# Kernel tuning notes

Measured on AMD Instinct MI355X. Metric: run time of the kernel, lower is better.

## Reference

```python
import jax, jax.numpy as jnp
import numpy as np

EPS = 1e-12  # torch F.normalize default eps


def setup_inputs() -> dict:
    key = jax.random.key(0)
    k1, k2, k3 = jax.random.split(key, 3)
    ns, d_in, n_feat, n_classes = 16384, 512, 256, 1000
    x = jax.random.normal(k1, (ns, d_in), dtype=jnp.float32)
    W = jax.random.normal(k2, (d_in, n_feat), dtype=jnp.float32) * 0.05
    # class prototypes: L2-normalized embeddings, one per seen class (seen_c == n_classes)
    means = jax.random.normal(k3, (n_classes, n_feat), dtype=jnp.float32)
    means = means / jnp.maximum(jnp.linalg.norm(means, axis=1, keepdims=True), EPS)
    return {"x": x, "W": W, "means": means, "t": 0}


def reference(x, W, means, t):
    # forward_training: backbone + L2 normalization along feature dim
    feats = x @ W                                   # [ns, n_feat]
    preds = feats / jnp.maximum(jnp.linalg.norm(feats, axis=1, keepdims=True), EPS)
    # deployment forward: nearest prototype by negative dot product
    # original: per-sample dist = -means @ pred^T; dist.min(0) -> class index
    dist = -(preds @ means.T)                       # [ns, seen_c]
    classpred = jnp.argmin(dist, axis=1)            # first min on ties, matches torch
    n_classes = means.shape[0]
    out = jax.nn.one_hot(classpred, n_classes, dtype=jnp.float32)  # [ns, n_classes]
    return out
```

## Files before the change

kernel.cpp:

```cpp
#include <hip/hip_runtime.h>
#include <float.h>

#define NS   16384
#define K1   512
#define F    256
#define NC   1000
#define SPB  64
#define NTHR 512
#define NBLK (NS / SPB)


typedef _Float16 half8  __attribute__((ext_vector_type(8)));
typedef _Float16 half4v __attribute__((ext_vector_type(4)));
typedef float    float4v __attribute__((ext_vector_type(4)));

#define M_OFF 262144

#define PREP_BLKS 192
#define ZERO_BLKS 2048

__global__ void prep(const float* __restrict__ W, const float* __restrict__ means,
                     _Float16* __restrict__ ws, float* __restrict__ out) {
    const int bid = blockIdx.x;
    if (bid >= PREP_BLKS) {
        const size_t total4 = (size_t)NS * NC / 4;
        const float4v z4 = (float4v){0.f, 0.f, 0.f, 0.f};
        size_t base = (size_t)(bid - PREP_BLKS) * 2048 + threadIdx.x;
#pragma unroll
        for (int j = 0; j < 8; ++j) {
            size_t q = base + (size_t)j * 256;
            if (q < total4)
                __builtin_nontemporal_store(z4, reinterpret_cast<float4v*>(out) + q);
        }
        return;
    }
    int g = bid * blockDim.x + threadIdx.x;
    if (g < 16384) {
        int lane = g & 63, tile = g >> 6;
        int ks = tile >> 4, nt = tile & 15;
        int k0 = ks * 32 + (lane >> 4) * 8;
        int n  = nt * 16 + (lane & 15);
        half8 hv, lv;
#pragma unroll
        for (int j = 0; j < 8; ++j) {
            float v = W[(size_t)(k0 + j) * F + n] * 16.0f;
            _Float16 hi = (_Float16)v;
            hv[j] = hi;
            lv[j] = (_Float16)(v - (float)hi);
        }
        _Float16* d = ws + (size_t)tile * 1024 + (size_t)lane * 8;
        *reinterpret_cast<half8*>(d)       = hv;
        *reinterpret_cast<half8*>(d + 512) = lv;
    } else {
        int gm = g - 16384;
        int lane = gm & 63, tile = gm >> 6;
        int ks = tile >> 6, gt = tile & 63;
        int k0 = ks * 32 + (lane >> 4) * 8;
        int c  = gt * 16 + (lane & 15);
        half8 hv, lv;
#pragma unroll
        for (int j = 0; j < 8; ++j) {
            float v = (c < NC) ? means[(size_t)c * F + k0 + j] * 16.0f : 0.0f;
            _Float16 hi = (_Float16)v;
            hv[j] = hi;
            lv[j] = (_Float16)(v - (float)hi);
        }
        _Float16* d = ws + M_OFF + (size_t)tile * 1024 + (size_t)lane * 8;
        *reinterpret_cast<half8*>(d)       = hv;
        *reinterpret_cast<half8*>(d + 512) = lv;
    }
}

#define MFMA(a, b, c) __builtin_amdgcn_mfma_f32_16x16x32_f16((a), (b), (c), 0, 0, 0)

__device__ __forceinline__ void vmwait(int n) {
    switch (n) {
        case 0: asm volatile("s_waitcnt vmcnt(0)" ::: "memory"); break;
        case 2: asm volatile("s_waitcnt vmcnt(2)" ::: "memory"); break;
        case 4: asm volatile("s_waitcnt vmcnt(4)" ::: "memory"); break;
        default: asm volatile("s_waitcnt vmcnt(6)" ::: "memory"); break;
    }
    __builtin_amdgcn_sched_barrier(0);
}

#define FH_OFF  0
#define FL_OFF  16384
#define OVL_OFF 32768
#define SH_HALVES 65536

#define FH_P(r, c) (&SH[FH_OFF + ((r) << 8) + ((c) ^ (((r) & 7) << 3))])
#define FL_P(r, c) (&SH[FL_OFF + ((r) << 8) + ((c) ^ (((r) & 7) << 3))])
#define XS_IDX(r, c) ((((r) >> 1) << 6) + ((((((r) & 1) << 5)) + (c)) ^ ((((r) >> 1) & 7) << 3)))
#define XSH_P(b, r, c) (&SH[OVL_OFF + (b) * 2048 + XS_IDX(r, c)])
#define XSL_P(b, r, c) (&SH[OVL_OFF + 4096 + (b) * 2048 + XS_IDX(r, c)])

__attribute__((amdgpu_flat_work_group_size(NTHR, NTHR), amdgpu_waves_per_eu(2, 4)))
__global__ void fused_mfma(const float* __restrict__ x,
                           const _Float16* __restrict__ ws,
                           float* __restrict__ out) {
    __shared__ _Float16 SH[SH_HALVES];
    __shared__ float cand_v[64][8];
    __shared__ int   cand_i[64][8];
    __shared__ int   bidx[64];

    const int tid  = threadIdx.x;
    const int lane = tid & 63;
    const int w    = tid >> 6;
    const int quad = lane >> 4;
    const int cl   = lane & 15;
    const int s0   = blockIdx.x * SPB;

    const int xrow = tid >> 3;
    const int xc4  = (tid & 7) * 4;

    float4v acc1[2][4];
#pragma unroll
    for (int p = 0; p < 2; ++p)
#pragma unroll
        for (int mt = 0; mt < 4; ++mt)
            acc1[p][mt] = (float4v){0.f, 0.f, 0.f, 0.f};

    const _Float16* wsrc = ws + ((size_t)(w * 2) << 10) + ((size_t)lane << 3);
    half8 wbh[2][2], wbl[2][2];
#pragma unroll
    for (int p = 0; p < 2; ++p) {
        wbh[0][p] = *reinterpret_cast<const half8*>(wsrc + p * 1024);
        wbl[0][p] = *reinterpret_cast<const half8*>(wsrc + p * 1024 + 512);
    }

    float4v xv = *reinterpret_cast<const float4v*>(x + (size_t)(s0 + xrow) * K1 + xc4);

#define P1_BODY(k, buf) do {                                                   \
        { half4v hx, lx;                                                       \
          _Pragma("unroll") for (int j = 0; j < 4; ++j) {                      \
              float v = xv[j] * 8.0f; _Float16 hi = (_Float16)v;               \
              hx[j] = hi; lx[j] = (_Float16)(v - (float)hi); }                 \
          *reinterpret_cast<half4v*>(XSH_P(buf, xrow, xc4)) = hx;              \
          *reinterpret_cast<half4v*>(XSL_P(buf, xrow, xc4)) = lx; }            \
        __syncthreads();                                                       \
        if ((k) < 15)                                                          \
            xv = *reinterpret_cast<const float4v*>(                            \
                x + (size_t)(s0 + xrow) * K1 + ((k) + 1) * 32 + xc4);          \
        _Pragma("unroll") for (int p = 0; p < 2; ++p) {                        \
            wbh[(buf) ^ 1][p] = *reinterpret_cast<const half8*>(               \
                wsrc + (size_t)((k) + 1) * 16384 + p * 1024);                  \
            wbl[(buf) ^ 1][p] = *reinterpret_cast<const half8*>(               \
                wsrc + (size_t)((k) + 1) * 16384 + p * 1024 + 512); }          \
        half8 ah[4], al[4];                                                    \
        _Pragma("unroll") for (int mt = 0; mt < 4; ++mt) {                     \
            ah[mt] = *reinterpret_cast<const half8*>(                          \
                XSH_P(buf, mt * 16 + cl, quad * 8));                           \
            al[mt] = *reinterpret_cast<const half8*>(                          \
                XSL_P(buf, mt * 16 + cl, quad * 8)); }                         \
        __builtin_amdgcn_s_setprio(1);                                         \
        _Pragma("unroll") for (int p = 0; p < 2; ++p)                          \
            _Pragma("unroll") for (int mt = 0; mt < 4; ++mt) {                 \
                acc1[p][mt] = MFMA(ah[mt], wbh[buf][p], acc1[p][mt]);          \
                acc1[p][mt] = MFMA(ah[mt], wbl[buf][p], acc1[p][mt]);          \
                acc1[p][mt] = MFMA(al[mt], wbh[buf][p], acc1[p][mt]); }        \
        __builtin_amdgcn_s_setprio(0);                                         \
    } while (0)

    for (int k2 = 0; k2 < 8; ++k2) {
        P1_BODY(2 * k2, 0);
        P1_BODY(2 * k2 + 1, 1);
    }

#pragma unroll
    for (int p = 0; p < 2; ++p)
#pragma unroll
        for (int mt = 0; mt < 4; ++mt)
#pragma unroll
            for (int r = 0; r < 4; ++r) {
                int srow = mt * 16 + quad * 4 + r;
                int n    = (w * 2 + p) * 16 + cl;
                float v  = acc1[p][mt][r];
                _Float16 hi = (_Float16)v;
                *FH_P(srow, n) = hi;
                *FL_P(srow, n) = (_Float16)(v - (float)hi);
            }
    __syncthreads();

    float4v acc2[4][8];
#pragma unroll
    for (int mt = 0; mt < 4; ++mt)
#pragma unroll
        for (int c = 0; c < 8; ++c)
            acc2[mt][c] = (float4v){0.f, 0.f, 0.f, 0.f};

    _Float16* fifo = &SH[OVL_OFF + w * 4096];
    const _Float16* mg = ws + M_OFF + ((size_t)w << 10) + ((size_t)lane << 3);

#define STAGE_OFF(goff, slot) do {                                             \
        __builtin_amdgcn_global_load_lds(                                      \
            (const __attribute__((address_space(1))) void*)(mg + (goff)),      \
            (__attribute__((address_space(3))) void*)(fifo + (slot) * 1024),   \
            16, 0, 0);                                                         \
        __builtin_amdgcn_global_load_lds(                                      \
            (const __attribute__((address_space(1))) void*)(mg + (goff) + 512),\
            (__attribute__((address_space(3))) void*)(fifo + (slot) * 1024 + 512),\
            16, 0, 0);                                                         \
    } while (0)

#define LOAD_A(kk) do { int c0_ = (kk) * 32 + quad * 8;                        \
        _Pragma("unroll") for (int mt = 0; mt < 4; ++mt) {                     \
            fah[mt] = *reinterpret_cast<const half8*>(FH_P(mt * 16 + cl, c0_));\
            fal[mt] = *reinterpret_cast<const half8*>(FL_P(mt * 16 + cl, c0_));\
        } } while (0)

#define FB_READ(slot, rb) do {                                                 \
        const _Float16* sl_ = fifo + (slot) * 1024 + lane * 8;                 \
        fbh[rb] = *reinterpret_cast<const half8*>(sl_);                        \
        fbl[rb] = *reinterpret_cast<const half8*>(sl_ + 512);                  \
    } while (0)

#define MFMA12(gt, rb) do {                                                    \
        __builtin_amdgcn_s_setprio(1);                                         \
        _Pragma("unroll") for (int mt = 0; mt < 4; ++mt) {                     \
            acc2[mt][gt] = MFMA(fah[mt], fbh[rb], acc2[mt][gt]);               \
            acc2[mt][gt] = MFMA(fah[mt], fbl[rb], acc2[mt][gt]);               \
            acc2[mt][gt] = MFMA(fal[mt], fbh[rb], acc2[mt][gt]); }             \
        __builtin_amdgcn_s_setprio(0);                                         \
    } while (0)

    half8 fah[4], fal[4];
    half8 fbh[2], fbl[2];

    STAGE_OFF(0, 0); STAGE_OFF(8192, 1); STAGE_OFF(16384, 2);
    LOAD_A(0);
    vmwait(4);
    FB_READ(0, 0);

    for (int ks = 0; ks < 7; ++ks) {
#pragma unroll
        for (int gt = 0; gt < 8; ++gt) {
            if (gt < 5) STAGE_OFF((gt + 3) * 8192, (gt + 3) & 3);
            else        STAGE_OFF(65536 + (gt - 5) * 8192, (gt + 3) & 3);
            if (gt == 0 && ks > 0) LOAD_A(ks);
            vmwait(4);
            FB_READ((gt + 1) & 3, (gt + 1) & 1);
            MFMA12(gt, gt & 1);
        }
        mg += 65536;
    }
#pragma unroll
    for (int gt = 0; gt < 8; ++gt) {
        if (gt < 5) STAGE_OFF((gt + 3) * 8192, (gt + 3) & 3);
        if (gt == 0) LOAD_A(7);
        if (gt < 5)       vmwait(4);
        else if (gt == 5) vmwait(2);
        else if (gt == 6) vmwait(0);
        if (gt < 7) FB_READ((gt + 1) & 3, (gt + 1) & 1);
        MFMA12(gt, gt & 1);
    }

#pragma unroll
    for (int mt = 0; mt < 4; ++mt)
#pragma unroll
        for (int r = 0; r < 4; ++r) {
            float v  = -FLT_MAX;
            int   ix = 0x7FFFFFFF;
#pragma unroll
            for (int nt = 0; nt < 8; ++nt) {
                int c = (nt * 8 + w) * 16 + cl;
                if (c < NC) {
                    float sc = acc2[mt][nt][r];
                    if (sc > v) { v = sc; ix = c; }
                }
            }
#pragma unroll
            for (int off = 1; off < 16; off <<= 1) {
                float ov = __shfl_xor(v, off, 64);
                int   oi = __shfl_xor(ix, off, 64);
                if (ov > v || (ov == v && oi < ix)) { v = ov; ix = oi; }
            }
            if (cl == 0) {
                int srow = mt * 16 + quad * 4 + r;
                cand_v[srow][w] = v;
                cand_i[srow][w] = ix;
            }
        }
    __syncthreads();

    if (tid < SPB) {
        float v  = cand_v[tid][0];
        int   ix = cand_i[tid][0];
#pragma unroll
        for (int q = 1; q < 8; ++q) {
            float ov = cand_v[tid][q];
            int   oi = cand_i[tid][q];
            if (ov > v || (ov == v && oi < ix)) { v = ov; ix = oi; }
        }
        bidx[tid] = ix;
    }
    __syncthreads();

    if (tid < SPB)
        out[(size_t)(s0 + tid) * NC + bidx[tid]] = 1.0f;
}

extern "C" void kernel_launch(void* const* d_in, const int* in_sizes, int n_in,
                              void* d_out, int out_size, void* d_ws, size_t ws_size,
                              hipStream_t stream) {
    const float* x     = (const float*)d_in[0];
    const float* W     = (const float*)d_in[1];
    const float* means = (const float*)d_in[2];
    float* out         = (float*)d_out;
    _Float16* ws       = (_Float16*)d_ws;

    prep<<<PREP_BLKS + ZERO_BLKS, 256, 0, stream>>>(W, means, ws, out);
    fused_mfma<<<NBLK, NTHR, 0, stream>>>(x, ws, out);
}
```

Measured before the change: 138.5 us.

## Stage x in half-K chunks and restructure prototype pipeline with barriers

Phase 1 now loads and converts half of each x row (256 columns) into a larger swizzled LDS tile at once, so the per-k-step __syncthreads goes away and only one extra barrier per half remains. Phase 2 replaces the 4-slot per-wave FIFO with a double buffer holding two column tiles per stage. Each stage is bracketed by s_barrier so the waves stay in lockstep. The aim is to cut synchronization and the number of load-wait steps. The risks are a shallower prefetch depth and added workgroup-wide barriers in phase 2.

```diff
diff --git a/kernel.cpp b/kernel.cpp
--- a/kernel.cpp
+++ b/kernel.cpp
@@ -90,9 +90,8 @@
 
 #define FH_P(r, c) (&SH[FH_OFF + ((r) << 8) + ((c) ^ (((r) & 7) << 3))])
 #define FL_P(r, c) (&SH[FL_OFF + ((r) << 8) + ((c) ^ (((r) & 7) << 3))])
-#define XS_IDX(r, c) ((((r) >> 1) << 6) + ((((((r) & 1) << 5)) + (c)) ^ ((((r) >> 1) & 7) << 3)))
-#define XSH_P(b, r, c) (&SH[OVL_OFF + (b) * 2048 + XS_IDX(r, c)])
-#define XSL_P(b, r, c) (&SH[OVL_OFF + 4096 + (b) * 2048 + XS_IDX(r, c)])
+#define XH_P(r, c) (&SH[OVL_OFF + ((r) << 8) + ((c) ^ (((r) & 7) << 3))])
+#define XL_P(r, c) (&SH[OVL_OFF + 16384 + ((r) << 8) + ((c) ^ (((r) & 7) << 3))])
 
 __attribute__((amdgpu_flat_work_group_size(NTHR, NTHR), amdgpu_waves_per_eu(2, 4)))
 __global__ void fused_mfma(const float* __restrict__ x,
@@ -111,7 +110,7 @@
     const int s0   = blockIdx.x * SPB;
 
     const int xrow = tid >> 3;
-    const int xc4  = (tid & 7) * 4;
+    const int xk0  = (tid & 7) * 32;
 
     float4v acc1[2][4];
 #pragma unroll
@@ -128,42 +127,56 @@
         wbl[0][p] = *reinterpret_cast<const half8*>(wsrc + p * 1024 + 512);
     }
 
-    float4v xv = *reinterpret_cast<const float4v*>(x + (size_t)(s0 + xrow) * K1 + xc4);
-
-#define P1_BODY(k, buf) do {                                                   \
-        { half4v hx, lx;                                                       \
-          _Pragma("unroll") for (int j = 0; j < 4; ++j) {                      \
-              float v = xv[j] * 8.0f; _Float16 hi = (_Float16)v;               \
-              hx[j] = hi; lx[j] = (_Float16)(v - (float)hi); }                 \
-          *reinterpret_cast<half4v*>(XSH_P(buf, xrow, xc4)) = hx;              \
-          *reinterpret_cast<half4v*>(XSL_P(buf, xrow, xc4)) = lx; }            \
-        __syncthreads();                                                       \
-        if ((k) < 15)                                                          \
-            xv = *reinterpret_cast<const float4v*>(                            \
-                x + (size_t)(s0 + xrow) * K1 + ((k) + 1) * 32 + xc4);          \
-        _Pragma("unroll") for (int p = 0; p < 2; ++p) {                        \
-            wbh[(buf) ^ 1][p] = *reinterpret_cast<const half8*>(               \
-                wsrc + (size_t)((k) + 1) * 16384 + p * 1024);                  \
-            wbl[(buf) ^ 1][p] = *reinterpret_cast<const half8*>(               \
-                wsrc + (size_t)((k) + 1) * 16384 + p * 1024 + 512); }          \
+#define P1B(ksl, par) do {                                                     \
+        const int ks_ = h * 8 + (ksl);                                         \
+        if (ks_ < 15) {                                                        \
+            _Pragma("unroll") for (int p = 0; p < 2; ++p) {                    \
+                wbh[(par) ^ 1][p] = *reinterpret_cast<const half8*>(           \
+                    wsrc + (size_t)(ks_ + 1) * 16384 + p * 1024);              \
+                wbl[(par) ^ 1][p] = *reinterpret_cast<const half8*>(           \
+                    wsrc + (size_t)(ks_ + 1) * 16384 + p * 1024 + 512); } }    \
         half8 ah[4], al[4];                                                    \
         _Pragma("unroll") for (int mt = 0; mt < 4; ++mt) {                     \
             ah[mt] = *reinterpret_cast<const half8*>(                          \
-                XSH_P(buf, mt * 16 + cl, quad * 8));                           \
+                XH_P(mt * 16 + cl, (ksl) * 32 + quad * 8));                    \
             al[mt] = *reinterpret_cast<const half8*>(                          \
-                XSL_P(buf, mt * 16 + cl, quad * 8)); }                         \
+                XL_P(mt * 16 + cl, (ksl) * 32 + quad * 8)); }                  \
         __builtin_amdgcn_s_setprio(1);                                         \
         _Pragma("unroll") for (int p = 0; p < 2; ++p)                          \
             _Pragma("unroll") for (int mt = 0; mt < 4; ++mt) {                 \
-                acc1[p][mt] = MFMA(ah[mt], wbh[buf][p], acc1[p][mt]);          \
-                acc1[p][mt] = MFMA(ah[mt], wbl[buf][p], acc1[p][mt]);          \
-                acc1[p][mt] = MFMA(al[mt], wbh[buf][p], acc1[p][mt]); }        \
+                acc1[p][mt] = MFMA(ah[mt], wbh[par][p], acc1[p][mt]);          \
+                acc1[p][mt] = MFMA(ah[mt], wbl[par][p], acc1[p][mt]);          \
+                acc1[p][mt] = MFMA(al[mt], wbh[par][p], acc1[p][mt]); }        \
         __builtin_amdgcn_s_setprio(0);                                         \
     } while (0)
 
-    for (int k2 = 0; k2 < 8; ++k2) {
-        P1_BODY(2 * k2, 0);
-        P1_BODY(2 * k2 + 1, 1);
+    for (int h = 0; h < 2; ++h) {
+        if (h) __syncthreads();
+        {
+            const float* xp = x + (size_t)(s0 + xrow) * K1 + h * 256 + xk0;
+            float4v xv[8];
+#pragma unroll
+            for (int j = 0; j < 8; ++j)
+                xv[j] = *reinterpret_cast<const float4v*>(xp + j * 4);
+#pragma unroll
+            for (int j8 = 0; j8 < 4; ++j8) {
+                half8 hx, lx;
+#pragma unroll
+                for (int e = 0; e < 8; ++e) {
+                    float v = xv[j8 * 2 + (e >> 2)][e & 3] * 8.0f;
+                    _Float16 hi = (_Float16)v;
+                    hx[e] = hi;
+                    lx[e] = (_Float16)(v - (float)hi);
+                }
+                *reinterpret_cast<half8*>(XH_P(xrow, xk0 + j8 * 8)) = hx;
+                *reinterpret_cast<half8*>(XL_P(xrow, xk0 + j8 * 8)) = lx;
+            }
+        }
+        __syncthreads();
+        for (int k2 = 0; k2 < 4; ++k2) {
+            P1B(2 * k2, 0);
+            P1B(2 * k2 + 1, 1);
+        }
     }
 
 #pragma unroll
@@ -191,14 +204,14 @@
     _Float16* fifo = &SH[OVL_OFF + w * 4096];
     const _Float16* mg = ws + M_OFF + ((size_t)w << 10) + ((size_t)lane << 3);
 
-#define STAGE_OFF(goff, slot) do {                                             \
+#define STAGE2(goff, loff) do {                                                \
         __builtin_amdgcn_global_load_lds(                                      \
             (const __attribute__((address_space(1))) void*)(mg + (goff)),      \
-            (__attribute__((address_space(3))) void*)(fifo + (slot) * 1024),   \
+            (__attribute__((address_space(3))) void*)(fifo + (loff)),          \
             16, 0, 0);                                                         \
         __builtin_amdgcn_global_load_lds(                                      \
             (const __attribute__((address_space(1))) void*)(mg + (goff) + 512),\
-            (__attribute__((address_space(3))) void*)(fifo + (slot) * 1024 + 512),\
+            (__attribute__((address_space(3))) void*)(fifo + (loff) + 512),    \
             16, 0, 0);                                                         \
     } while (0)
 
@@ -208,50 +221,47 @@
             fal[mt] = *reinterpret_cast<const half8*>(FL_P(mt * 16 + cl, c0_));\
         } } while (0)
 
-#define FB_READ(slot, rb) do {                                                 \
-        const _Float16* sl_ = fifo + (slot) * 1024 + lane * 8;                 \
-        fbh[rb] = *reinterpret_cast<const half8*>(sl_);                        \
-        fbl[rb] = *reinterpret_cast<const half8*>(sl_ + 512);                  \
+#define MFMA12(gt, BH, BL) do {                                                \
+        _Pragma("unroll") for (int mt = 0; mt < 4; ++mt) {                     \
+            acc2[mt][gt] = MFMA(fah[mt], BH, acc2[mt][gt]);                    \
+            acc2[mt][gt] = MFMA(fah[mt], BL, acc2[mt][gt]);                    \
+            acc2[mt][gt] = MFMA(fal[mt], BH, acc2[mt][gt]); }                  \
     } while (0)
 
-#define MFMA12(gt, rb) do {                                                    \
+#define P2B(j4) do {                                                           \
+        if ((j4) < 3) {                                                        \
+            STAGE2((((j4) + 1) * 2)     * 8192, (((j4) + 1) & 1) * 2048);      \
+            STAGE2((((j4) + 1) * 2 + 1) * 8192, (((j4) + 1) & 1) * 2048 + 1024);\
+            vmwait(4);                                                         \
+        } else if (ks < 7) {                                                   \
+            STAGE2(65536,        (((j4) + 1) & 1) * 2048);                     \
+            STAGE2(65536 + 8192, (((j4) + 1) & 1) * 2048 + 1024);              \
+            vmwait(4);                                                         \
+        } else {                                                               \
+            vmwait(0);                                                         \
+        }                                                                      \
+        const _Float16* sl_ = fifo + ((j4) & 1) * 2048 + (size_t)lane * 8;     \
+        half8 b0h = *reinterpret_cast<const half8*>(sl_);                      \
+        half8 b0l = *reinterpret_cast<const half8*>(sl_ + 512);                \
+        half8 b1h = *reinterpret_cast<const half8*>(sl_ + 1024);               \
+        half8 b1l = *reinterpret_cast<const half8*>(sl_ + 1536);               \
+        if ((j4) == 0) LOAD_A(ks);                                             \
+        __builtin_amdgcn_s_barrier();                                          \
         __builtin_amdgcn_s_setprio(1);                                         \
-        _Pragma("unroll") for (int mt = 0; mt < 4; ++mt) {                     \
-            acc2[mt][gt] = MFMA(fah[mt], fbh[rb], acc2[mt][gt]);               \
-            acc2[mt][gt] = MFMA(fah[mt], fbl[rb], acc2[mt][gt]);               \
-            acc2[mt][gt] = MFMA(fal[mt], fbh[rb], acc2[mt][gt]); }             \
+        MFMA12((j4) * 2,     b0h, b0l);                                        \
+        MFMA12((j4) * 2 + 1, b1h, b1l);                                        \
         __builtin_amdgcn_s_setprio(0);                                         \
+        __builtin_amdgcn_s_barrier();                                          \
     } while (0)
 
     half8 fah[4], fal[4];
-    half8 fbh[2], fbl[2];
-
-    STAGE_OFF(0, 0); STAGE_OFF(8192, 1); STAGE_OFF(16384, 2);
-    LOAD_A(0);
-    vmwait(4);
-    FB_READ(0, 0);
-
-    for (int ks = 0; ks < 7; ++ks) {
-#pragma unroll
-        for (int gt = 0; gt < 8; ++gt) {
-            if (gt < 5) STAGE_OFF((gt + 3) * 8192, (gt + 3) & 3);
-            else        STAGE_OFF(65536 + (gt - 5) * 8192, (gt + 3) & 3);
-            if (gt == 0 && ks > 0) LOAD_A(ks);
-            vmwait(4);
-            FB_READ((gt + 1) & 3, (gt + 1) & 1);
-            MFMA12(gt, gt & 1);
-        }
+
+    STAGE2(0, 0);
+    STAGE2(8192, 1024);
+
+    for (int ks = 0; ks < 8; ++ks) {
+        P2B(0); P2B(1); P2B(2); P2B(3);
         mg += 65536;
-    }
-#pragma unroll
-    for (int gt = 0; gt < 8; ++gt) {
-        if (gt < 5) STAGE_OFF((gt + 3) * 8192, (gt + 3) & 3);
-        if (gt == 0) LOAD_A(7);
-        if (gt < 5)       vmwait(4);
-        else if (gt == 5) vmwait(2);
-        else if (gt == 6) vmwait(0);
-        if (gt < 7) FB_READ((gt + 1) & 3, (gt + 1) & 1);
-        MFMA12(gt, gt & 1);
     }
 
 #pragma unroll
```

Result: no change. 139.5 us (+0.7%).

## Use single-fp16 prototype GEMM with error-bounded top-2 rescoring of ambiguous rows

Applied to the files above, without the earlier changes.

The second GEMM against the class prototypes drops the three-MFMA hi/lo split and uses only the fp16-hi parts, cutting its MFMA count and staged bytes by two thirds. To keep the argmax exact, it tracks the top two scores per row and derives an error bound from the feature norm. Rows whose margin falls below that bound get their candidate classes rescored in fp32 against the original means. This adds top-2 tracking, shared-memory worklists and a fallback pass, and the fixed error constant or the worklist capacity could miss ties in rare cases.

```diff
diff --git a/kernel.cpp b/kernel.cpp
--- a/kernel.cpp
+++ b/kernel.cpp
@@ -1,5 +1,6 @@
 #include <hip/hip_runtime.h>
 #include <float.h>
+#include <math.h>
 
 #define NS   16384
 #define K1   512
@@ -76,7 +77,9 @@
 __device__ __forceinline__ void vmwait(int n) {
     switch (n) {
         case 0: asm volatile("s_waitcnt vmcnt(0)" ::: "memory"); break;
+        case 1: asm volatile("s_waitcnt vmcnt(1)" ::: "memory"); break;
         case 2: asm volatile("s_waitcnt vmcnt(2)" ::: "memory"); break;
+        case 3: asm volatile("s_waitcnt vmcnt(3)" ::: "memory"); break;
         case 4: asm volatile("s_waitcnt vmcnt(4)" ::: "memory"); break;
         default: asm volatile("s_waitcnt vmcnt(6)" ::: "memory"); break;
     }
@@ -94,14 +97,24 @@
 #define XSH_P(b, r, c) (&SH[OVL_OFF + (b) * 2048 + XS_IDX(r, c)])
 #define XSL_P(b, r, c) (&SH[OVL_OFF + 4096 + (b) * 2048 + XS_IDX(r, c)])
 
+#define WLCAP 768
+
 __attribute__((amdgpu_flat_work_group_size(NTHR, NTHR), amdgpu_waves_per_eu(2, 4)))
 __global__ void fused_mfma(const float* __restrict__ x,
                            const _Float16* __restrict__ ws,
+                           const float* __restrict__ means,
                            float* __restrict__ out) {
     __shared__ _Float16 SH[SH_HALVES];
     __shared__ float cand_v[64][8];
     __shared__ int   cand_i[64][8];
+    __shared__ float cand_v2[64][8];
+    __shared__ float norm_p[64][8];
+    __shared__ float thrE[64];
+    __shared__ int   ambR[64];
     __shared__ int   bidx[64];
+    __shared__ int   wl[WLCAP];
+    __shared__ float wls[WLCAP];
+    __shared__ int   wlcnt;
 
     const int tid  = threadIdx.x;
     const int lane = tid & 63;
@@ -112,6 +125,8 @@
 
     const int xrow = tid >> 3;
     const int xc4  = (tid & 7) * 4;
+
+    if (tid == 0) wlcnt = 0;
 
     float4v acc1[2][4];
 #pragma unroll
@@ -141,11 +156,12 @@
         if ((k) < 15)                                                          \
             xv = *reinterpret_cast<const float4v*>(                            \
                 x + (size_t)(s0 + xrow) * K1 + ((k) + 1) * 32 + xc4);          \
-        _Pragma("unroll") for (int p = 0; p < 2; ++p) {                        \
-            wbh[(buf) ^ 1][p] = *reinterpret_cast<const half8*>(               \
-                wsrc + (size_t)((k) + 1) * 16384 + p * 1024);                  \
-            wbl[(buf) ^ 1][p] = *reinterpret_cast<const half8*>(               \
-                wsrc + (size_t)((k) + 1) * 16384 + p * 1024 + 512); }          \
+        if ((k) < 15) {                                                        \
+            _Pragma("unroll") for (int p = 0; p < 2; ++p) {                    \
+                wbh[(buf) ^ 1][p] = *reinterpret_cast<const half8*>(           \
+                    wsrc + (size_t)((k) + 1) * 16384 + p * 1024);              \
+                wbl[(buf) ^ 1][p] = *reinterpret_cast<const half8*>(           \
+                    wsrc + (size_t)((k) + 1) * 16384 + p * 1024 + 512); } }    \
         half8 ah[4], al[4];                                                    \
         _Pragma("unroll") for (int mt = 0; mt < 4; ++mt) {                     \
             ah[mt] = *reinterpret_cast<const half8*>(                          \
@@ -167,18 +183,26 @@
     }
 
 #pragma unroll
-    for (int p = 0; p < 2; ++p)
-#pragma unroll
-        for (int mt = 0; mt < 4; ++mt)
-#pragma unroll
-            for (int r = 0; r < 4; ++r) {
-                int srow = mt * 16 + quad * 4 + r;
-                int n    = (w * 2 + p) * 16 + cl;
-                float v  = acc1[p][mt][r];
+    for (int mt = 0; mt < 4; ++mt)
+#pragma unroll
+        for (int r = 0; r < 4; ++r) {
+            const int srow = mt * 16 + quad * 4 + r;
+            float s2 = 0.f;
+#pragma unroll
+            for (int p = 0; p < 2; ++p) {
+                int n   = (w * 2 + p) * 16 + cl;
+                float v = acc1[p][mt][r];
                 _Float16 hi = (_Float16)v;
                 *FH_P(srow, n) = hi;
                 *FL_P(srow, n) = (_Float16)(v - (float)hi);
-            }
+                float hf = (float)hi;
+                s2 = fmaf(hf, hf, s2);
+            }
+#pragma unroll
+            for (int off = 1; off < 16; off <<= 1)
+                s2 += __shfl_xor(s2, off, 64);
+            if (cl == 0) norm_p[srow][w] = s2;
+        }
     __syncthreads();
 
     float4v acc2[4][8];
@@ -191,107 +215,163 @@
     _Float16* fifo = &SH[OVL_OFF + w * 4096];
     const _Float16* mg = ws + M_OFF + ((size_t)w << 10) + ((size_t)lane << 3);
 
-#define STAGE_OFF(goff, slot) do {                                             \
-        __builtin_amdgcn_global_load_lds(                                      \
-            (const __attribute__((address_space(1))) void*)(mg + (goff)),      \
-            (__attribute__((address_space(3))) void*)(fifo + (slot) * 1024),   \
-            16, 0, 0);                                                         \
-        __builtin_amdgcn_global_load_lds(                                      \
-            (const __attribute__((address_space(1))) void*)(mg + (goff) + 512),\
-            (__attribute__((address_space(3))) void*)(fifo + (slot) * 1024 + 512),\
-            16, 0, 0);                                                         \
+#define MOFF(i) ((size_t)(((i) >> 3) * 65536 + ((i) & 7) * 8192))
+#define STAGE1(i) __builtin_amdgcn_global_load_lds(                            \
+        (const __attribute__((address_space(1))) void*)(mg + MOFF(i)),         \
+        (__attribute__((address_space(3))) void*)(fifo + ((i) & 7) * 512),     \
+        16, 0, 0)
+#define LOAD_A(kk, DST) do { const int c0_ = (kk) * 32 + quad * 8;             \
+        _Pragma("unroll") for (int mt = 0; mt < 4; ++mt)                       \
+            DST[mt] = *reinterpret_cast<const half8*>(                         \
+                FH_P(mt * 16 + cl, c0_));                                      \
     } while (0)
 
-#define LOAD_A(kk) do { int c0_ = (kk) * 32 + quad * 8;                        \
-        _Pragma("unroll") for (int mt = 0; mt < 4; ++mt) {                     \
-            fah[mt] = *reinterpret_cast<const half8*>(FH_P(mt * 16 + cl, c0_));\
-            fal[mt] = *reinterpret_cast<const half8*>(FL_P(mt * 16 + cl, c0_));\
-        } } while (0)
-
-#define FB_READ(slot, rb) do {                                                 \
-        const _Float16* sl_ = fifo + (slot) * 1024 + lane * 8;                 \
-        fbh[rb] = *reinterpret_cast<const half8*>(sl_);                        \
-        fbl[rb] = *reinterpret_cast<const half8*>(sl_ + 512);                  \
-    } while (0)
-
-#define MFMA12(gt, rb) do {                                                    \
-        __builtin_amdgcn_s_setprio(1);                                         \
-        _Pragma("unroll") for (int mt = 0; mt < 4; ++mt) {                     \
-            acc2[mt][gt] = MFMA(fah[mt], fbh[rb], acc2[mt][gt]);               \
-            acc2[mt][gt] = MFMA(fah[mt], fbl[rb], acc2[mt][gt]);               \
-            acc2[mt][gt] = MFMA(fal[mt], fbh[rb], acc2[mt][gt]); }             \
-        __builtin_amdgcn_s_setprio(0);                                         \
-    } while (0)
-
-    half8 fah[4], fal[4];
-    half8 fbh[2], fbl[2];
-
-    STAGE_OFF(0, 0); STAGE_OFF(8192, 1); STAGE_OFF(16384, 2);
-    LOAD_A(0);
-    vmwait(4);
-    FB_READ(0, 0);
-
-    for (int ks = 0; ks < 7; ++ks) {
-#pragma unroll
-        for (int gt = 0; gt < 8; ++gt) {
-            if (gt < 5) STAGE_OFF((gt + 3) * 8192, (gt + 3) & 3);
-            else        STAGE_OFF(65536 + (gt - 5) * 8192, (gt + 3) & 3);
-            if (gt == 0 && ks > 0) LOAD_A(ks);
-            vmwait(4);
-            FB_READ((gt + 1) & 3, (gt + 1) & 1);
-            MFMA12(gt, gt & 1);
-        }
-        mg += 65536;
-    }
-#pragma unroll
-    for (int gt = 0; gt < 8; ++gt) {
-        if (gt < 5) STAGE_OFF((gt + 3) * 8192, (gt + 3) & 3);
-        if (gt == 0) LOAD_A(7);
-        if (gt < 5)       vmwait(4);
-        else if (gt == 5) vmwait(2);
-        else if (gt == 6) vmwait(0);
-        if (gt < 7) FB_READ((gt + 1) & 3, (gt + 1) & 1);
-        MFMA12(gt, gt & 1);
+    half8 fahA[4], fahB[4];
+    half8 fbh[2];
+
+    STAGE1(0); STAGE1(1); STAGE1(2); STAGE1(3);
+    LOAD_A(0, fahA);
+    vmwait(3);
+    fbh[0] = *reinterpret_cast<const half8*>(fifo + (size_t)lane * 8);
+
+#pragma unroll
+    for (int i = 0; i < 64; ++i) {
+        if (i < 60) STAGE1(i + 4);
+        if (i < 60)      vmwait(3);
+        else if (i == 60) vmwait(2);
+        else if (i == 61) vmwait(1);
+        else if (i == 62) vmwait(0);
+        if (i < 63)
+            fbh[(i + 1) & 1] = *reinterpret_cast<const half8*>(
+                fifo + ((i + 1) & 7) * 512 + (size_t)lane * 8);
+        if ((i & 7) == 6 && i < 56) {
+            if (((i >> 3) + 1) & 1) LOAD_A((i >> 3) + 1, fahB);
+            else                    LOAD_A((i >> 3) + 1, fahA);
+        }
+        const int gt = i & 7, rb = i & 1;
+        __builtin_amdgcn_s_setprio(1);
+        if ((i >> 3) & 1) {
+#pragma unroll
+            for (int mt = 0; mt < 4; ++mt)
+                acc2[mt][gt] = MFMA(fahB[mt], fbh[rb], acc2[mt][gt]);
+        } else {
+#pragma unroll
+            for (int mt = 0; mt < 4; ++mt)
+                acc2[mt][gt] = MFMA(fahA[mt], fbh[rb], acc2[mt][gt]);
+        }
+        __builtin_amdgcn_s_setprio(0);
     }
 
 #pragma unroll
     for (int mt = 0; mt < 4; ++mt)
 #pragma unroll
         for (int r = 0; r < 4; ++r) {
-            float v  = -FLT_MAX;
-            int   ix = 0x7FFFFFFF;
+            float v1 = -FLT_MAX, v2 = -FLT_MAX;
+            int   i1 = 0x7FFFFFFF;
 #pragma unroll
             for (int nt = 0; nt < 8; ++nt) {
                 int c = (nt * 8 + w) * 16 + cl;
                 if (c < NC) {
                     float sc = acc2[mt][nt][r];
-                    if (sc > v) { v = sc; ix = c; }
+                    if (sc > v1) { v2 = v1; v1 = sc; i1 = c; }
+                    else if (sc > v2) v2 = sc;
                 }
             }
 #pragma unroll
             for (int off = 1; off < 16; off <<= 1) {
-                float ov = __shfl_xor(v, off, 64);
-                int   oi = __shfl_xor(ix, off, 64);
-                if (ov > v || (ov == v && oi < ix)) { v = ov; ix = oi; }
+                float ov1 = __shfl_xor(v1, off, 64);
+                int   oi1 = __shfl_xor(i1, off, 64);
+                float ov2 = __shfl_xor(v2, off, 64);
+                if (ov1 > v1 || (ov1 == v1 && oi1 < i1)) {
+                    v2 = fmaxf(v1, ov2); v1 = ov1; i1 = oi1;
+                } else {
+                    v2 = fmaxf(v2, ov1);
+                }
             }
             if (cl == 0) {
                 int srow = mt * 16 + quad * 4 + r;
-                cand_v[srow][w] = v;
-                cand_i[srow][w] = ix;
+                cand_v[srow][w]  = v1;
+                cand_i[srow][w]  = i1;
+                cand_v2[srow][w] = v2;
             }
         }
     __syncthreads();
 
     if (tid < SPB) {
-        float v  = cand_v[tid][0];
-        int   ix = cand_i[tid][0];
+        float v1 = cand_v[tid][0], v2 = cand_v2[tid][0];
+        int   i1 = cand_i[tid][0];
+        float ns = norm_p[tid][0];
 #pragma unroll
         for (int q = 1; q < 8; ++q) {
-            float ov = cand_v[tid][q];
-            int   oi = cand_i[tid][q];
-            if (ov > v || (ov == v && oi < ix)) { v = ov; ix = oi; }
-        }
-        bidx[tid] = ix;
+            float ov1 = cand_v[tid][q], ov2 = cand_v2[tid][q];
+            int   oi1 = cand_i[tid][q];
+            ns += norm_p[tid][q];
+            if (ov1 > v1 || (ov1 == v1 && oi1 < i1)) {
+                v2 = fmaxf(v1, ov2); v1 = ov1; i1 = oi1;
+            } else {
+                v2 = fmaxf(v2, ov1);
+            }
+        }
+        float E2 = 0.03290f * sqrtf(ns);
+        bidx[tid] = i1;
+        ambR[tid] = (v1 - v2 < E2) ? 1 : 0;
+        thrE[tid] = v1 - E2;
+    }
+    __syncthreads();
+
+#pragma unroll
+    for (int mt = 0; mt < 4; ++mt)
+#pragma unroll
+        for (int r = 0; r < 4; ++r) {
+            const int row = mt * 16 + quad * 4 + r;
+            if (ambR[row]) {
+                const float th = thrE[row];
+#pragma unroll
+                for (int nt = 0; nt < 8; ++nt) {
+                    int c = (nt * 8 + w) * 16 + cl;
+                    if (c < NC && acc2[mt][nt][r] >= th) {
+                        int idx = atomicAdd(&wlcnt, 1);
+                        if (idx < WLCAP) wl[idx] = (row << 10) | c;
+                    }
+                }
+            }
+        }
+    __syncthreads();
+
+    {
+        int n = wlcnt < WLCAP ? wlcnt : WLCAP;
+        for (int e = w; e < n; e += 8) {
+            int rc = wl[e];
+            int row = rc >> 10, c = rc & 1023;
+            const float* mrow = means + (size_t)c * F;
+            int k = lane * 4;
+            float s = 0.f;
+#pragma unroll
+            for (int j = 0; j < 4; ++j) {
+                float f = (float)*FH_P(row, k + j) + (float)*FL_P(row, k + j);
+                s = fmaf(f, 16.0f * mrow[k + j], s);
+            }
+#pragma unroll
+            for (int off = 1; off < 64; off <<= 1)
+                s += __shfl_xor(s, off, 64);
+            if (lane == 0) wls[e] = s;
+        }
+    }
+    __syncthreads();
+
+    if (tid < SPB && ambR[tid]) {
+        int n = wlcnt < WLCAP ? wlcnt : WLCAP;
+        float best = -FLT_MAX;
+        int   bc   = 0x7FFFFFFF;
+        for (int e = 0; e < n; ++e) {
+            int rc = wl[e];
+            if ((rc >> 10) == tid) {
+                float s = wls[e];
+                int   c = rc & 1023;
+                if (s > best || (s == best && c < bc)) { best = s; bc = c; }
+            }
+        }
+        if (bc != 0x7FFFFFFF) bidx[tid] = bc;
     }
     __syncthreads();
 
@@ -309,5 +389,5 @@
     _Float16* ws       = (_Float16*)d_ws;
 
     prep<<<PREP_BLKS + ZERO_BLKS, 256, 0, stream>>>(W, means, ws, out);
-    fused_mfma<<<NBLK, NTHR, 0, stream>>>(x, ws, out);
+    fused_mfma<<<NBLK, NTHR, 0, stream>>>(x, ws, means, out);
 }
```

Result: slower. 142.4 us (+2.8%).
